# Kernel tuning notes

Measured on AMD Instinct MI355X. Metric: run time of the kernel, lower is better.

The kernel has to match this reference:

```python
import jax, jax.numpy as jnp
import numpy as np

N_TRAJ = 4096
T = 128
LAT = 64          # latent_dim
NDATA = 64        # n_data_dim (values half of input)
INP = 2 * NDATA   # input_dim = values + mask
NGRU = 100        # gate hidden units
NODE = 100        # ode-func hidden units
TZ = 100          # transform_z0 hidden units


def setup_inputs() -> dict:
    key = jax.random.key(0)
    ks = jax.random.split(key, 16)
    vals = jax.random.normal(ks[0], (N_TRAJ, T, NDATA), jnp.float32)
    mask = (jax.random.uniform(ks[1], (N_TRAJ, T, NDATA)) > 0.5).astype(jnp.float32)
    data = jnp.concatenate([vals * mask, mask], axis=-1)  # [values | mask]
    tps = jnp.linspace(0.0, 2.0, T).astype(jnp.float32)   # uniform -> Euler branch every step
    D = 2 * LAT + INP
    def lin(k, i, o):
        return jax.random.normal(k, (i, o), jnp.float32) * 0.1
    return {
        "data": data, "tps": tps,
        "ug_w1": lin(ks[2], D, NGRU), "ug_b1": jnp.zeros(NGRU, jnp.float32),
        "ug_w2": lin(ks[3], NGRU, LAT), "ug_b2": jnp.zeros(LAT, jnp.float32),
        "rg_w1": lin(ks[4], D, NGRU), "rg_b1": jnp.zeros(NGRU, jnp.float32),
        "rg_w2": lin(ks[5], NGRU, LAT), "rg_b2": jnp.zeros(LAT, jnp.float32),
        "ns_w1": lin(ks[6], D, NGRU), "ns_b1": jnp.zeros(NGRU, jnp.float32),
        "ns_w2": lin(ks[7], NGRU, 2 * LAT), "ns_b2": jnp.zeros(2 * LAT, jnp.float32),
        "ode_w1": lin(ks[8], LAT, NODE), "ode_b1": jnp.zeros(NODE, jnp.float32),
        "ode_w2": lin(ks[9], NODE, LAT), "ode_b2": jnp.zeros(LAT, jnp.float32),
        "tz_w1": lin(ks[10], 2 * LAT, TZ), "tz_b1": jnp.zeros(TZ, jnp.float32),
        "tz_w2": lin(ks[11], TZ, 2 * LAT), "tz_b2": jnp.zeros(2 * LAT, jnp.float32),
    }


def reference(data, tps, ug_w1, ug_b1, ug_w2, ug_b2, rg_w1, rg_b1, rg_w2, rg_b2,
              ns_w1, ns_b1, ns_w2, ns_b2, ode_w1, ode_b1, ode_w2, ode_b2,
              tz_w1, tz_b1, tz_w2, tz_b2):
    n_traj = data.shape[0]

    def mlp2(x, w1, b1, w2, b2):
        return jnp.tanh(x @ w1 + b1) @ w2 + b2

    def gru(y_mu, y_std, x):
        yc = jnp.concatenate([y_mu, y_std, x], axis=-1)
        u = jax.nn.sigmoid(mlp2(yc, ug_w1, ug_b1, ug_w2, ug_b2))
        r = jax.nn.sigmoid(mlp2(yc, rg_w1, rg_b1, rg_w2, rg_b2))
        ns = mlp2(jnp.concatenate([y_mu * r, y_std * r, x], axis=-1),
                  ns_w1, ns_b1, ns_w2, ns_b2)
        new_state = ns[..., :LAT]
        new_std = jnp.abs(ns[..., LAT:])
        new_y = (1.0 - u) * new_state + u * y_mu
        new_y_std = (1.0 - u) * new_std + u * y_std
        m = x[..., NDATA:]  # mask half
        new_y = m * new_y + (1.0 - m) * y_mu
        new_y_std = m * new_y_std + (1.0 - m) * y_std
        return new_y, jnp.abs(new_y_std)

    # run_backwards=True: iterate i = T-1 .. 0
    xs = data[:, ::-1, :].transpose(1, 0, 2)       # (T, n_traj, INP)
    rev = tps[::-1]                                 # [t_{T-1}, ..., t_0]
    # first Euler dt = tps[-1] - (tps[-1] + 0.01) = -0.01; then dt_k = t_i - t_{i+1}
    dts = jnp.concatenate([jnp.full((1,), -0.01, jnp.float32), rev[1:] - rev[:-1]])

    def step(carry, inp):
        y, s = carry
        x, dt = inp
        y_ode = y + mlp2(y, ode_w1, ode_b1, ode_w2, ode_b2) * dt  # single Euler step
        y, s = gru(y_ode, s, x)
        return (y, s), None

    y0 = jnp.zeros((n_traj, LAT), data.dtype)
    (yi, yi_std), _ = jax.lax.scan(step, (y0, y0), (xs, dts))

    z = mlp2(jnp.concatenate([yi, yi_std], axis=-1), tz_w1, tz_b1, tz_w2, tz_b2)
    z0_mu = z[..., :LAT]
    z0_std = jnp.abs(z[..., LAT:])
    return z0_mu[None], z0_std[None]  # (1, n_traj, z0_dim) each
```

## Files before the change

kernel.cpp:

```cpp
#include <hip/hip_runtime.h>

typedef unsigned short u16;
typedef __attribute__((ext_vector_type(8))) short s8;
typedef __attribute__((ext_vector_type(4))) short s4;
typedef __attribute__((ext_vector_type(4))) float f4;

#define N_TRAJ 4096
#define TSTEPS 128
#define LATD   64
#define INPD   128

#define OB1 0
#define OB2 128
#define UB1 192
#define UB2 320
#define RB1 384
#define RB2 512
#define NB1 576
#define NB2 704
#define TB1 832
#define TB2 960
#define DTS 1088
#define NBIAS 1216

#define OFF_UG1 0
#define OFF_RG1 32768
#define OFF_NS1 65536
#define OFF_OD1 98304
#define OFF_UG2 106496
#define OFF_RG2 114688
#define OFF_NS2 122880
#define OFF_OD2 139264
#define OFF_TZ1 147456
#define OFF_TZ2 163840
#define PACK_ELEMS 180224

#define SYO 68

__device__ u16 g_pack[PACK_ELEMS];
__device__ float g_bias[NBIAS];

__device__ __forceinline__ float b2f(u16 u) {
    union { unsigned int i; float f; } v; v.i = ((unsigned int)u) << 16; return v.f;
}
__device__ __forceinline__ u16 f2b(float f) {
    unsigned int x = __float_as_uint(f);
    unsigned int r = (x + 0x7FFFu + ((x >> 16) & 1u)) >> 16;
    return (u16)r;
}
__device__ __forceinline__ unsigned int cvtpk(float lo, float hi) {
    unsigned int r;
    asm("v_cvt_pk_bf16_f32 %0, %1, %2" : "=v"(r) : "v"(lo), "v"(hi));
    return r;
}
__device__ __forceinline__ int is_f32(const void* tps) {
    return (*(const unsigned int*)tps) == 0u;
}
__device__ __forceinline__ float rdany(const void* a, int i, int isf32) {
    return isf32 ? ((const float*)a)[i] : b2f(((const u16*)a)[i]);
}
__device__ __forceinline__ float sigm(float x) {
    x = fminf(fmaxf(x, -30.f), 30.f);
    float e = __expf(-x);
    return __builtin_amdgcn_rcpf(1.f + e);
}
__device__ __forceinline__ float tanh_(float x) {
    x = fminf(fmaxf(x, -15.f), 15.f);
    float e = __expf(-2.f * x);
    return (1.f - e) * __builtin_amdgcn_rcpf(1.f + e);
}

__device__ __forceinline__ s8 aread(const u16* buf, int lane, int ks) {
    int row = lane & 15;
    int b = (ks << 6) + ((lane >> 4) << 4);
    int off = (row << 8) + (b ^ ((row & 7) << 4));
    return *(const s8*)((const char*)buf + off);
}
__device__ __forceinline__ void hwrite4(u16* buf, int traj, int ncol0, float a, float b, float c, float d) {
    int off = (traj << 8) + ((ncol0 << 1) ^ ((traj & 7) << 4));
    uint2 v;
    v.x = cvtpk(a, b);
    v.y = cvtpk(c, d);
    *(uint2*)((char*)buf + off) = v;
}
__device__ __forceinline__ s4 sread4(const u16* buf, int traj, int col0) {
    int off = (traj << 8) + ((col0 << 1) ^ ((traj & 7) << 4));
    return *(const s4*)((const char*)buf + off);
}
__device__ __forceinline__ s4 load_x4(const void* data, size_t elemIdx, int isf32) {
    s4 r;
    if (isf32) {
        f4 v = *(const f4*)((const float*)data + elemIdx);
#pragma unroll
        for (int j = 0; j < 4; ++j) r[j] = (short)f2b(v[j]);
    } else {
        r = *(const s4*)((const u16*)data + elemIdx);
    }
    return r;
}

struct PackP {
    const void* src[10];
    const void* tps;
    int Kr[10], Nr[10], KS[10], sz[10];
};

__global__ __launch_bounds__(256) void repack_kernel(PackP p) {
    int gid = blockIdx.x * 256 + threadIdx.x;
    if (gid >= PACK_ELEMS) return;
    int isf32 = is_f32(p.tps);
    int idx = gid, m = 0, base = 0;
    while (m < 10 && idx >= p.sz[m]) { idx -= p.sz[m]; base += p.sz[m]; ++m; }
    if (m >= 10) return;
    int i = idx & 7;
    int l = (idx >> 3) & 63;
    int rest = idx >> 9;
    int ks = rest % p.KS[m];
    int nt = rest / p.KS[m];
    int k = ks * 32 + ((l >> 4) << 3) + i;
    int n = nt * 16 + (l & 15);
    u16 v = 0;
    if (k < p.Kr[m] && n < p.Nr[m]) v = f2b(rdany(p.src[m], k * p.Nr[m] + n, isf32));
    g_pack[base + idx] = v;
}

struct PrepP {
    const void *tps, *ob1, *ob2, *ub1, *ub2, *rb1, *rb2, *nb1, *nb2, *tb1, *tb2;
};

__global__ __launch_bounds__(256) void prep_bias(PrepP p) {
    int isf32 = is_f32(p.tps);
    int tid = threadIdx.x;
    for (int i = tid; i < 128; i += 256) {
        g_bias[OB1 + i] = (i < 100) ? rdany(p.ob1, i, isf32) : 0.f;
        g_bias[UB1 + i] = (i < 100) ? rdany(p.ub1, i, isf32) : 0.f;
        g_bias[RB1 + i] = (i < 100) ? rdany(p.rb1, i, isf32) : 0.f;
        g_bias[NB1 + i] = (i < 100) ? rdany(p.nb1, i, isf32) : 0.f;
        g_bias[TB1 + i] = (i < 100) ? rdany(p.tb1, i, isf32) : 0.f;
        g_bias[NB2 + i] = rdany(p.nb2, i, isf32);
        g_bias[TB2 + i] = rdany(p.tb2, i, isf32);
        g_bias[DTS + i] = (i == 0) ? -0.01f
                                   : (rdany(p.tps, 127 - i, isf32) - rdany(p.tps, 128 - i, isf32));
    }
    for (int i = tid; i < 64; i += 256) {
        g_bias[OB2 + i] = rdany(p.ob2, i, isf32);
        g_bias[UB2 + i] = rdany(p.ub2, i, isf32);
        g_bias[RB2 + i] = rdany(p.rb2, i, isf32);
    }
}

struct MainP {
    const void *data, *tps;
    void* out;
};

#define WLOAD(off, KSn, nt, ks) (*(const s8*)(pk + (off) + (((((nt) * (KSn)) + (ks)) << 6) + lane) * 8))
#define MFMA(wf, af, c) __builtin_amdgcn_mfma_f32_16x16x32_bf16((wf), (af), (c), 0, 0, 0)

__global__ __launch_bounds__(512, 2) void enc_main(MainP p) {
    __shared__ u16 s_x[2][2048];
    __shared__ u16 s_yc[2048];
    __shared__ u16 s_yc2[2048];
    __shared__ u16 s_hA[2048];
    __shared__ u16 s_hB[2048];
    __shared__ float s_yo[16 * SYO];
    __shared__ float s_u[16 * SYO];
    __shared__ float s_b[NBIAS];

    int tid = threadIdx.x, lane = tid & 63, w = tid >> 6;
    int btraj = blockIdx.x << 4;
    const u16* pk = g_pack;
    int isf32 = is_f32(p.tps);

    for (int i = tid; i < NBIAS; i += 512) s_b[i] = g_bias[i];
    for (int i = tid; i < 2048; i += 512) s_yc[i] = 0;

    s8 wl1u[8], wl1r[8], wl1n[8];
    s8 wod1[2];
    s8 wod2[4], w2x[4], wn2[4];
#pragma unroll
    for (int ks = 0; ks < 8; ++ks) {
        wl1u[ks] = WLOAD(OFF_UG1, 8, w, ks);
        wl1r[ks] = WLOAD(OFF_RG1, 8, w, ks);
        wl1n[ks] = WLOAD(OFF_NS1, 8, w, ks);
    }
    wod1[0] = WLOAD(OFF_OD1, 2, w, 0);
    wod1[1] = WLOAD(OFF_OD1, 2, w, 1);
#pragma unroll
    for (int ks = 0; ks < 4; ++ks) {
        wod2[ks] = WLOAD(OFF_OD2, 4, (w & 3), ks);
        wn2[ks] = WLOAD(OFF_NS2, 4, w, ks);
    }
    if (w < 4) {
#pragma unroll
        for (int ks = 0; ks < 4; ++ks) w2x[ks] = WLOAD(OFF_UG2, 4, w, ks);
    } else {
#pragma unroll
        for (int ks = 0; ks < 4; ++ks) w2x[ks] = WLOAD(OFF_RG2, 4, w - 4, ks);
    }

    f4 ymu_r = {0.f, 0.f, 0.f, 0.f};
    f4 s_r = {0.f, 0.f, 0.f, 0.f};
    f4 yo_r = {0.f, 0.f, 0.f, 0.f};
    f4 u_r = {0.f, 0.f, 0.f, 0.f};

    int xrow = tid >> 5, xk = tid & 31;
    int xoff = (xrow << 8) + ((xk << 3) ^ ((xrow & 7) << 4));
    {
        s4 xr = load_x4(p.data, ((size_t)(btraj + xrow) * TSTEPS + 127) * INPD + (xk << 2), isf32);
        *(s4*)((char*)s_x[0] + xoff) = xr;
    }
    __syncthreads();

    const f4 zero4 = {0.f, 0.f, 0.f, 0.f};
    int traj = lane & 15;
    int nbase = (w << 4) + ((lane >> 4) << 2);

    for (int it = 0; it < TSTEPS; ++it) {
        int cur = it & 1;
        float dt = s_b[DTS + it];

        s4 xnext;
        if (it < 127) {
            xnext = load_x4(p.data, ((size_t)(btraj + xrow) * TSTEPS + (126 - it)) * INPD + (xk << 2), isf32);
        }

        f4 au0 = zero4, au1 = zero4, ar0 = zero4, ar1 = zero4;
        f4 an0 = zero4, an1 = zero4;
        s8 ax0, ax1, ax2, ax3;

        {
            ax0 = aread(s_x[cur], lane, 0);
            ax1 = aread(s_x[cur], lane, 1);
            ax2 = aread(s_x[cur], lane, 2);
            ax3 = aread(s_x[cur], lane, 3);
            s8 ay0 = aread(s_yc, lane, 0);
            s8 ay1 = aread(s_yc, lane, 1);
            s8 ay2 = aread(s_yc, lane, 2);
            s8 ay3 = aread(s_yc, lane, 3);
            f4 ao = zero4;
            ao = MFMA(wod1[0], ay0, ao);
            ao = MFMA(wod1[1], ay1, ao);
            au0 = MFMA(wl1u[2], ay2, au0);
            ar0 = MFMA(wl1r[2], ay2, ar0);
            au0 = MFMA(wl1u[3], ay3, au0);
            ar0 = MFMA(wl1r[3], ay3, ar0);
            au0 = MFMA(wl1u[4], ax0, au0);
            ar0 = MFMA(wl1r[4], ax0, ar0);
            au0 = MFMA(wl1u[5], ax1, au0);
            ar0 = MFMA(wl1r[5], ax1, ar0);
            au1 = MFMA(wl1u[6], ax2, au1);
            ar1 = MFMA(wl1r[6], ax2, ar1);
            au1 = MFMA(wl1u[7], ax3, au1);
            ar1 = MFMA(wl1r[7], ax3, ar1);
            f4 b4 = *(const f4*)(s_b + OB1 + nbase);
            hwrite4(s_hA, traj, nbase, tanh_(ao[0] + b4[0]), tanh_(ao[1] + b4[1]),
                    tanh_(ao[2] + b4[2]), tanh_(ao[3] + b4[3]));
        }
        __syncthreads();

        if (w < 4) {
            f4 ac0 = zero4, ac1 = zero4;
            ac0 = MFMA(wod2[0], aread(s_hA, lane, 0), ac0);
            ac1 = MFMA(wod2[2], aread(s_hA, lane, 2), ac1);
            ac0 = MFMA(wod2[1], aread(s_hA, lane, 1), ac0);
            ac1 = MFMA(wod2[3], aread(s_hA, lane, 3), ac1);
            f4 b4 = *(const f4*)(s_b + OB2 + nbase);
#pragma unroll
            for (int j = 0; j < 4; ++j) yo_r[j] = ymu_r[j] + (ac0[j] + ac1[j] + b4[j]) * dt;
            *(f4*)(s_yo + traj * SYO + nbase) = yo_r;
            hwrite4(s_yc, traj, nbase, yo_r[0], yo_r[1], yo_r[2], yo_r[3]);
        } else {
            an0 = MFMA(wl1n[4], ax0, an0);
            an1 = MFMA(wl1n[6], ax2, an1);
            an0 = MFMA(wl1n[5], ax1, an0);
            an1 = MFMA(wl1n[7], ax3, an1);
        }
        __syncthreads();

        {
            s8 a0 = aread(s_yc, lane, 0);
            s8 a1 = aread(s_yc, lane, 1);
            au1 = MFMA(wl1u[0], a0, au1);
            ar1 = MFMA(wl1r[0], a0, ar1);
            au1 = MFMA(wl1u[1], a1, au1);
            ar1 = MFMA(wl1r[1], a1, ar1);
            f4 bu4 = *(const f4*)(s_b + UB1 + nbase);
            f4 br4 = *(const f4*)(s_b + RB1 + nbase);
            hwrite4(s_hA, traj, nbase,
                    tanh_(au0[0] + au1[0] + bu4[0]), tanh_(au0[1] + au1[1] + bu4[1]),
                    tanh_(au0[2] + au1[2] + bu4[2]), tanh_(au0[3] + au1[3] + bu4[3]));
            hwrite4(s_hB, traj, nbase,
                    tanh_(ar0[0] + ar1[0] + br4[0]), tanh_(ar0[1] + ar1[1] + br4[1]),
                    tanh_(ar0[2] + ar1[2] + br4[2]), tanh_(ar0[3] + ar1[3] + br4[3]));
        }
        __syncthreads();

        if (w < 4) {
            an0 = MFMA(wl1n[4], ax0, an0);
            an1 = MFMA(wl1n[6], ax2, an1);
            an0 = MFMA(wl1n[5], ax1, an0);
            an1 = MFMA(wl1n[7], ax3, an1);
            f4 uac0 = zero4, uac1 = zero4;
            uac0 = MFMA(w2x[0], aread(s_hA, lane, 0), uac0);
            uac1 = MFMA(w2x[2], aread(s_hA, lane, 2), uac1);
            uac0 = MFMA(w2x[1], aread(s_hA, lane, 1), uac0);
            uac1 = MFMA(w2x[3], aread(s_hA, lane, 3), uac1);
            f4 b4 = *(const f4*)(s_b + UB2 + nbase);
#pragma unroll
            for (int j = 0; j < 4; ++j) u_r[j] = sigm(uac0[j] + uac1[j] + b4[j]);
            *(f4*)(s_u + traj * SYO + nbase) = u_r;
        } else {
            f4 rac0 = zero4, rac1 = zero4;
            rac0 = MFMA(w2x[0], aread(s_hB, lane, 0), rac0);
            rac1 = MFMA(w2x[2], aread(s_hB, lane, 2), rac1);
            rac0 = MFMA(w2x[1], aread(s_hB, lane, 1), rac0);
            rac1 = MFMA(w2x[3], aread(s_hB, lane, 3), rac1);
            int sb = nbase - 64;
            f4 b4 = *(const f4*)(s_b + RB2 + sb);
            f4 yo4 = *(const f4*)(s_yo + traj * SYO + sb);
            f4 rv;
#pragma unroll
            for (int j = 0; j < 4; ++j) rv[j] = sigm(rac0[j] + rac1[j] + b4[j]);
            hwrite4(s_yc2, traj, sb, yo4[0] * rv[0], yo4[1] * rv[1], yo4[2] * rv[2], yo4[3] * rv[3]);
            hwrite4(s_yc2, traj, nbase, s_r[0] * rv[0], s_r[1] * rv[1], s_r[2] * rv[2], s_r[3] * rv[3]);
        }
        __syncthreads();

        {
            an0 = MFMA(wl1n[0], aread(s_yc2, lane, 0), an0);
            an1 = MFMA(wl1n[2], aread(s_yc2, lane, 2), an1);
            an0 = MFMA(wl1n[1], aread(s_yc2, lane, 1), an0);
            an1 = MFMA(wl1n[3], aread(s_yc2, lane, 3), an1);
            f4 b4 = *(const f4*)(s_b + NB1 + nbase);
            hwrite4(s_hA, traj, nbase,
                    tanh_(an0[0] + an1[0] + b4[0]), tanh_(an0[1] + an1[1] + b4[1]),
                    tanh_(an0[2] + an1[2] + b4[2]), tanh_(an0[3] + an1[3] + b4[3]));
        }
        __syncthreads();

        {
            f4 fn0 = zero4, fn1 = zero4;
            fn0 = MFMA(wn2[0], aread(s_hA, lane, 0), fn0);
            fn1 = MFMA(wn2[2], aread(s_hA, lane, 2), fn1);
            fn0 = MFMA(wn2[1], aread(s_hA, lane, 1), fn0);
            fn1 = MFMA(wn2[3], aread(s_hA, lane, 3), fn1);
            if (it < 127) *(s4*)((char*)s_x[cur ^ 1] + xoff) = xnext;

            f4 b4 = *(const f4*)(s_b + NB2 + nbase);
            if (w < 4) {
                s4 mm = sread4(s_x[cur], traj, 64 + nbase);
#pragma unroll
                for (int j = 0; j < 4; ++j) {
                    float nsv = fn0[j] + fn1[j] + b4[j];
                    float m = b2f((u16)mm[j]);
                    float mg = m * (1.f - u_r[j]);
                    ymu_r[j] = yo_r[j] + mg * (nsv - yo_r[j]);
                }
                hwrite4(s_yc, traj, nbase, ymu_r[0], ymu_r[1], ymu_r[2], ymu_r[3]);
            } else {
                int sb = nbase - 64;
                s4 mm = sread4(s_x[cur], traj, nbase);
                f4 u4 = *(const f4*)(s_u + traj * SYO + sb);
#pragma unroll
                for (int j = 0; j < 4; ++j) {
                    float nsv = fabsf(fn0[j] + fn1[j] + b4[j]);
                    float m = b2f((u16)mm[j]);
                    float mg = m * (1.f - u4[j]);
                    float nss = s_r[j] + mg * (nsv - s_r[j]);
                    s_r[j] = fabsf(nss);
                }
                hwrite4(s_yc, traj, nbase, s_r[0], s_r[1], s_r[2], s_r[3]);
            }
        }
        __syncthreads();
    }

    s8 wt1[4], wt2[4];
#pragma unroll
    for (int ks = 0; ks < 4; ++ks) {
        wt1[ks] = WLOAD(OFF_TZ1, 4, w, ks);
        wt2[ks] = WLOAD(OFF_TZ2, 4, w, ks);
    }
    {
        f4 t1 = zero4;
#pragma unroll
        for (int ks = 0; ks < 4; ++ks) t1 = MFMA(wt1[ks], aread(s_yc, lane, ks), t1);
        f4 b4 = *(const f4*)(s_b + TB1 + nbase);
        hwrite4(s_hA, traj, nbase, tanh_(t1[0] + b4[0]), tanh_(t1[1] + b4[1]),
                tanh_(t1[2] + b4[2]), tanh_(t1[3] + b4[3]));
    }
    __syncthreads();
    {
        f4 t2 = zero4;
#pragma unroll
        for (int ks = 0; ks < 4; ++ks) t2 = MFMA(wt2[ks], aread(s_hA, lane, ks), t2);
        f4 b4 = *(const f4*)(s_b + TB2 + nbase);
        int gtraj = btraj + traj;
        f4 z;
        size_t base;
        if (w < 4) {
#pragma unroll
            for (int j = 0; j < 4; ++j) z[j] = t2[j] + b4[j];
            base = (size_t)gtraj * 64 + nbase;
        } else {
#pragma unroll
            for (int j = 0; j < 4; ++j) z[j] = fabsf(t2[j] + b4[j]);
            base = (size_t)N_TRAJ * 64 + (size_t)gtraj * 64 + (nbase - 64);
        }
        if (isf32) {
            *(f4*)((float*)p.out + base) = z;
        } else {
            uint2 pv;
            pv.x = cvtpk(z[0], z[1]);
            pv.y = cvtpk(z[2], z[3]);
            *(uint2*)((u16*)p.out + base) = pv;
        }
    }
}

extern "C" void kernel_launch(void* const* d_in, const int* in_sizes, int n_in,
                              void* d_out, int out_size, void* d_ws, size_t ws_size,
                              hipStream_t stream) {
    PackP pp;
    const int srcIdx[10] = {2, 6, 10, 14, 4, 8, 12, 16, 18, 20};
    const int Kr[10] = {256, 256, 256, 64, 100, 100, 100, 100, 128, 100};
    const int Nr[10] = {100, 100, 100, 100, 64, 64, 128, 64, 100, 128};
    const int KS[10] = {8, 8, 8, 2, 4, 4, 4, 4, 4, 4};
    const int NT[10] = {8, 8, 8, 8, 4, 4, 8, 4, 8, 8};
    for (int i = 0; i < 10; ++i) {
        pp.src[i] = d_in[srcIdx[i]];
        pp.Kr[i] = Kr[i];
        pp.Nr[i] = Nr[i];
        pp.KS[i] = KS[i];
        pp.sz[i] = KS[i] * NT[i] * 512;
    }
    pp.tps = d_in[1];
    repack_kernel<<<(PACK_ELEMS + 255) / 256, 256, 0, stream>>>(pp);

    PrepP bp;
    bp.tps = d_in[1];
    bp.ob1 = d_in[15]; bp.ob2 = d_in[17];
    bp.ub1 = d_in[3];  bp.ub2 = d_in[5];
    bp.rb1 = d_in[7];  bp.rb2 = d_in[9];
    bp.nb1 = d_in[11]; bp.nb2 = d_in[13];
    bp.tb1 = d_in[19]; bp.tb2 = d_in[21];
    prep_bias<<<1, 256, 0, stream>>>(bp);

    MainP mp;
    mp.data = d_in[0];
    mp.tps = d_in[1];
    mp.out = d_out;
    enc_main<<<N_TRAJ / 16, 512, 0, stream>>>(mp);
}
```

Measured before the change: 358.2 us.

## Software-pipeline x-input gate MFMAs into previous step's later phases

```diff
diff --git a/kernel.cpp b/kernel.cpp
--- a/kernel.cpp
+++ b/kernel.cpp
@@ -67,7 +67,7 @@
 __device__ __forceinline__ float tanh_(float x) {
     x = fminf(fmaxf(x, -15.f), 15.f);
     float e = __expf(-2.f * x);
-    return (1.f - e) * __builtin_amdgcn_rcpf(1.f + e);
+    return __builtin_fmaf(2.f, __builtin_amdgcn_rcpf(1.f + e), -1.f);
 }
 
 __device__ __forceinline__ s8 aread(const u16* buf, int lane, int ks) {
@@ -216,6 +216,20 @@
     int traj = lane & 15;
     int nbase = (w << 4) + ((lane >> 4) << 2);
 
+    s8 axc0 = aread(s_x[0], lane, 0);
+    s8 axc1 = aread(s_x[0], lane, 1);
+    s8 axc2 = aread(s_x[0], lane, 2);
+    s8 axc3 = aread(s_x[0], lane, 3);
+    f4 auA = zero4, arA = zero4;
+    auA = MFMA(wl1u[4], axc0, auA);
+    arA = MFMA(wl1r[4], axc0, arA);
+    auA = MFMA(wl1u[5], axc1, auA);
+    arA = MFMA(wl1r[5], axc1, arA);
+    auA = MFMA(wl1u[6], axc2, auA);
+    arA = MFMA(wl1r[6], axc2, arA);
+    auA = MFMA(wl1u[7], axc3, auA);
+    arA = MFMA(wl1r[7], axc3, arA);
+
     for (int it = 0; it < TSTEPS; ++it) {
         int cur = it & 1;
         float dt = s_b[DTS + it];
@@ -225,15 +239,9 @@
             xnext = load_x4(p.data, ((size_t)(btraj + xrow) * TSTEPS + (126 - it)) * INPD + (xk << 2), isf32);
         }
 
-        f4 au0 = zero4, au1 = zero4, ar0 = zero4, ar1 = zero4;
         f4 an0 = zero4, an1 = zero4;
-        s8 ax0, ax1, ax2, ax3;
 
         {
-            ax0 = aread(s_x[cur], lane, 0);
-            ax1 = aread(s_x[cur], lane, 1);
-            ax2 = aread(s_x[cur], lane, 2);
-            ax3 = aread(s_x[cur], lane, 3);
             s8 ay0 = aread(s_yc, lane, 0);
             s8 ay1 = aread(s_yc, lane, 1);
             s8 ay2 = aread(s_yc, lane, 2);
@@ -241,18 +249,10 @@
             f4 ao = zero4;
             ao = MFMA(wod1[0], ay0, ao);
             ao = MFMA(wod1[1], ay1, ao);
-            au0 = MFMA(wl1u[2], ay2, au0);
-            ar0 = MFMA(wl1r[2], ay2, ar0);
-            au0 = MFMA(wl1u[3], ay3, au0);
-            ar0 = MFMA(wl1r[3], ay3, ar0);
-            au0 = MFMA(wl1u[4], ax0, au0);
-            ar0 = MFMA(wl1r[4], ax0, ar0);
-            au0 = MFMA(wl1u[5], ax1, au0);
-            ar0 = MFMA(wl1r[5], ax1, ar0);
-            au1 = MFMA(wl1u[6], ax2, au1);
-            ar1 = MFMA(wl1r[6], ax2, ar1);
-            au1 = MFMA(wl1u[7], ax3, au1);
-            ar1 = MFMA(wl1r[7], ax3, ar1);
+            auA = MFMA(wl1u[2], ay2, auA);
+            arA = MFMA(wl1r[2], ay2, arA);
+            auA = MFMA(wl1u[3], ay3, auA);
+            arA = MFMA(wl1r[3], ay3, arA);
             f4 b4 = *(const f4*)(s_b + OB1 + nbase);
             hwrite4(s_hA, traj, nbase, tanh_(ao[0] + b4[0]), tanh_(ao[1] + b4[1]),
                     tanh_(ao[2] + b4[2]), tanh_(ao[3] + b4[3]));
@@ -271,36 +271,38 @@
             *(f4*)(s_yo + traj * SYO + nbase) = yo_r;
             hwrite4(s_yc, traj, nbase, yo_r[0], yo_r[1], yo_r[2], yo_r[3]);
         } else {
-            an0 = MFMA(wl1n[4], ax0, an0);
-            an1 = MFMA(wl1n[6], ax2, an1);
-            an0 = MFMA(wl1n[5], ax1, an0);
-            an1 = MFMA(wl1n[7], ax3, an1);
+            an0 = MFMA(wl1n[4], axc0, an0);
+            an1 = MFMA(wl1n[6], axc2, an1);
+            an0 = MFMA(wl1n[5], axc1, an0);
+            an1 = MFMA(wl1n[7], axc3, an1);
         }
         __syncthreads();
 
         {
             s8 a0 = aread(s_yc, lane, 0);
             s8 a1 = aread(s_yc, lane, 1);
+            f4 au1 = zero4, ar1 = zero4;
             au1 = MFMA(wl1u[0], a0, au1);
             ar1 = MFMA(wl1r[0], a0, ar1);
             au1 = MFMA(wl1u[1], a1, au1);
             ar1 = MFMA(wl1r[1], a1, ar1);
+            if (it < 127) *(s4*)((char*)s_x[cur ^ 1] + xoff) = xnext;
             f4 bu4 = *(const f4*)(s_b + UB1 + nbase);
             f4 br4 = *(const f4*)(s_b + RB1 + nbase);
             hwrite4(s_hA, traj, nbase,
-                    tanh_(au0[0] + au1[0] + bu4[0]), tanh_(au0[1] + au1[1] + bu4[1]),
-                    tanh_(au0[2] + au1[2] + bu4[2]), tanh_(au0[3] + au1[3] + bu4[3]));
+                    tanh_(auA[0] + au1[0] + bu4[0]), tanh_(auA[1] + au1[1] + bu4[1]),
+                    tanh_(auA[2] + au1[2] + bu4[2]), tanh_(auA[3] + au1[3] + bu4[3]));
             hwrite4(s_hB, traj, nbase,
-                    tanh_(ar0[0] + ar1[0] + br4[0]), tanh_(ar0[1] + ar1[1] + br4[1]),
-                    tanh_(ar0[2] + ar1[2] + br4[2]), tanh_(ar0[3] + ar1[3] + br4[3]));
+                    tanh_(arA[0] + ar1[0] + br4[0]), tanh_(arA[1] + ar1[1] + br4[1]),
+                    tanh_(arA[2] + ar1[2] + br4[2]), tanh_(arA[3] + ar1[3] + br4[3]));
         }
         __syncthreads();
 
         if (w < 4) {
-            an0 = MFMA(wl1n[4], ax0, an0);
-            an1 = MFMA(wl1n[6], ax2, an1);
-            an0 = MFMA(wl1n[5], ax1, an0);
-            an1 = MFMA(wl1n[7], ax3, an1);
+            an0 = MFMA(wl1n[4], axc0, an0);
+            an1 = MFMA(wl1n[6], axc2, an1);
+            an0 = MFMA(wl1n[5], axc1, an0);
+            an1 = MFMA(wl1n[7], axc3, an1);
             f4 uac0 = zero4, uac1 = zero4;
             uac0 = MFMA(w2x[0], aread(s_hA, lane, 0), uac0);
             uac1 = MFMA(w2x[2], aread(s_hA, lane, 2), uac1);
@@ -327,11 +329,21 @@
         }
         __syncthreads();
 
+        s8 axn0, axn1, axn2, axn3;
+        f4 auN = zero4, arN = zero4;
         {
             an0 = MFMA(wl1n[0], aread(s_yc2, lane, 0), an0);
             an1 = MFMA(wl1n[2], aread(s_yc2, lane, 2), an1);
             an0 = MFMA(wl1n[1], aread(s_yc2, lane, 1), an0);
             an1 = MFMA(wl1n[3], aread(s_yc2, lane, 3), an1);
+            if (it < 127) {
+                axn0 = aread(s_x[cur ^ 1], lane, 0);
+                axn1 = aread(s_x[cur ^ 1], lane, 1);
+                auN = MFMA(wl1u[4], axn0, auN);
+                arN = MFMA(wl1r[4], axn0, arN);
+                auN = MFMA(wl1u[5], axn1, auN);
+                arN = MFMA(wl1r[5], axn1, arN);
+            }
             f4 b4 = *(const f4*)(s_b + NB1 + nbase);
             hwrite4(s_hA, traj, nbase,
                     tanh_(an0[0] + an1[0] + b4[0]), tanh_(an0[1] + an1[1] + b4[1]),
@@ -345,7 +357,14 @@
             fn1 = MFMA(wn2[2], aread(s_hA, lane, 2), fn1);
             fn0 = MFMA(wn2[1], aread(s_hA, lane, 1), fn0);
             fn1 = MFMA(wn2[3], aread(s_hA, lane, 3), fn1);
-            if (it < 127) *(s4*)((char*)s_x[cur ^ 1] + xoff) = xnext;
+            if (it < 127) {
+                axn2 = aread(s_x[cur ^ 1], lane, 2);
+                axn3 = aread(s_x[cur ^ 1], lane, 3);
+                auN = MFMA(wl1u[6], axn2, auN);
+                arN = MFMA(wl1r[6], axn2, arN);
+                auN = MFMA(wl1u[7], axn3, auN);
+                arN = MFMA(wl1r[7], axn3, arN);
+            }
 
             f4 b4 = *(const f4*)(s_b + NB2 + nbase);
             if (w < 4) {
@@ -374,6 +393,15 @@
             }
         }
         __syncthreads();
+
+        if (it < 127) {
+            auA = auN;
+            arA = arN;
+            axc0 = axn0;
+            axc1 = axn1;
+            axc2 = axn2;
+            axc3 = axn3;
+        }
     }
 
     s8 wt1[4], wt2[4];
```

New measurement: 342.4 us. -4.4%, faster.
